# Kernel tuning notes

Measured on AMD Instinct MI355X. Metric: run time of the kernel, lower is better.

## Reference

```python
import jax, jax.numpy as jnp
import numpy as np

B, N, F_IN = 16, 2048, 6
NUM_CLASSES = 16


def _laplacian(x):
    # x: [B,N,F]; Gaussian adjacency from pairwise sq distances, then sym-normalized Laplacian
    sq = jnp.sum(x * x, axis=-1, keepdims=True)            # [B,N,1]
    d2 = sq - 2.0 * jnp.einsum('bnf,bmf->bnm', x, x) + jnp.swapaxes(sq, 1, 2)
    adj = jnp.exp(-d2)                                      # [B,N,N]
    dinv = 1.0 / jnp.sqrt(jnp.sum(adj, axis=-1))            # [B,N]
    return jnp.eye(N, dtype=x.dtype) - adj * dinv[:, :, None] * dinv[:, None, :]


def _cheb(x, L, W, b):
    # Chebyshev conv: W [K,Fin,Fout], recursion x_k = 2 L x_{k-1} - x_{k-2}
    K = W.shape[0]
    x0 = x
    out = jnp.einsum('bnf,fg->bng', x0, W[0])
    if K > 1:
        x1 = jnp.einsum('bnm,bmf->bnf', L, x0)
        out = out + jnp.einsum('bnf,fg->bng', x1, W[1])
        for k in range(2, K):
            x2 = 2.0 * jnp.einsum('bnm,bmf->bnf', L, x1) - x0
            out = out + jnp.einsum('bnf,fg->bng', x2, W[k])
            x0, x1 = x1, x2
    return out + b


def setup_inputs() -> dict:
    key = jax.random.key(0)
    ks = jax.random.split(key, 16)

    def w(k, shape, fan_in):
        return jax.random.normal(k, shape, dtype=jnp.float32) * (1.0 / np.sqrt(fan_in))

    inp = {
        'x': jax.random.normal(ks[0], (B, N, F_IN), dtype=jnp.float32),
        'cat': jax.random.randint(ks[1], (B, 1), 0, NUM_CLASSES),
        'W1': w(ks[2], (6, 22, 128), 22), 'b1': jnp.zeros((128,), jnp.float32),
        'W2': w(ks[3], (5, 128, 512), 128), 'b2': jnp.zeros((512,), jnp.float32),
        'W3': w(ks[4], (3, 512, 1024), 512), 'b3': jnp.zeros((1024,), jnp.float32),
        'fc1_w': w(ks[5], (1024, 512), 1024), 'fc1_b': jnp.zeros((512,), jnp.float32),
        'fc2_w': w(ks[6], (1024, 128), 1024), 'fc2_b': jnp.zeros((128,), jnp.float32),
        'fc3_w': w(ks[7], (128, 50), 128), 'fc3_b': jnp.zeros((50,), jnp.float32),
        'br0': jnp.zeros((1, 1, 128), jnp.float32),
        'br1': jnp.zeros((1, 1, 512), jnp.float32),
        'br2': jnp.zeros((1, 1, 1024), jnp.float32),
        'br3': jnp.zeros((1, 1, 512), jnp.float32),
        'br4': jnp.zeros((1, 1, 128), jnp.float32),
        'br5': jnp.zeros((1, 1, 50), jnp.float32),
    }
    return inp


def reference(x, cat, W1, b1, W2, b2, W3, b3, fc1_w, fc1_b, fc2_w, fc2_b,
              fc3_w, fc3_b, br0, br1, br2, br3, br4, br5):
    L = _laplacian(x)                                        # computed under no_grad in torch
    oh = jax.nn.one_hot(cat[:, 0], NUM_CLASSES, dtype=x.dtype)   # [B,16]
    cat_tiled = jnp.broadcast_to(oh[:, None, :], (x.shape[0], N, NUM_CLASSES))
    h = jnp.concatenate([x, cat_tiled], axis=2)              # [B,N,22]

    h = jax.nn.relu(_cheb(h, L, W1, b1) + br0)               # [B,N,128]
    h = jax.nn.relu(_cheb(h, L, W2, b2) + br1)               # [B,N,512]
    x1 = h
    h = jax.nn.relu(_cheb(h, L, W3, b3) + br2)               # [B,N,1024]

    h = jax.nn.relu(h @ fc1_w + fc1_b + br3)                 # [B,N,512]
    h = jnp.concatenate([h, x1], axis=2)                     # [B,N,1024]
    h = jax.nn.relu(h @ fc2_w + fc2_b + br4)                 # [B,N,128]
    h = jax.nn.relu(h @ fc3_w + fc3_b + br5)                 # [B,N,50]
    return h
```

## Files before the change

kernel.cpp:

```cpp
#include <hip/hip_runtime.h>

#define BB 16
#define NN 2048
#define FIN 6
#define MTOT (BB*NN)

typedef unsigned short u16;
typedef __attribute__((ext_vector_type(8))) short  short8;
typedef __attribute__((ext_vector_type(4))) float  f32x4;

__device__ inline float ldf(const u16* p) {
  unsigned u = ((unsigned)*p) << 16; float f; __builtin_memcpy(&f, &u, 4); return f;
}
__device__ inline u16 tobf(float v) {
  unsigned u; __builtin_memcpy(&u, &v, 4);
  u = (u + 0x7FFFu + ((u >> 16) & 1u)) >> 16;
  return (u16)u;
}
__device__ inline void stf(u16* p, float v) { *p = tobf(v); }

__device__ __forceinline__ void gload16(const u16* g, u16* l) {
  __builtin_amdgcn_global_load_lds(
      (const __attribute__((address_space(1))) void*)g,
      (__attribute__((address_space(3))) void*)l, 16, 0, 0);
}

__global__ __launch_bounds__(256) void k_dpart(const float* __restrict__ x,
                                               float* __restrict__ dsum) {
  __shared__ float xs[512][FIN];
  __shared__ float sqs[512];
  const int b = blockIdx.y;
  const int j0 = blockIdx.z * 512;
  const float* xb = x + (size_t)b * NN * FIN;
  for (int l = threadIdx.x; l < 512 * FIN; l += 256) ((float*)xs)[l] = xb[(size_t)j0 * FIN + l];
  __syncthreads();
  for (int j = threadIdx.x; j < 512; j += 256) {
    float s = 0.f;
#pragma unroll
    for (int f = 0; f < FIN; ++f) { float v = xs[j][f]; s = fmaf(v, v, s); }
    sqs[j] = s;
  }
  __syncthreads();
  const int i = blockIdx.x * 256 + threadIdx.x;
  float xi[FIN];
#pragma unroll
  for (int f = 0; f < FIN; ++f) xi[f] = xb[(size_t)i * FIN + f];
  float sqi = 0.f;
#pragma unroll
  for (int f = 0; f < FIN; ++f) sqi = fmaf(xi[f], xi[f], sqi);
  float a0 = 0.f, a1 = 0.f, a2 = 0.f, a3 = 0.f;
  for (int j = 0; j < 512; j += 4) {
#pragma unroll
    for (int u = 0; u < 4; ++u) {
      const int jj = j + u;
      float dot = 0.f;
#pragma unroll
      for (int f = 0; f < FIN; ++f) dot = fmaf(xs[jj][f], xi[f], dot);
      const float e = __expf(2.f * dot - sqi - sqs[jj]);
      if (u == 0) a0 += e; else if (u == 1) a1 += e; else if (u == 2) a2 += e; else a3 += e;
    }
  }
  atomicAdd(&dsum[b * NN + i], (a0 + a1) + (a2 + a3));
}

__global__ void k_rsq(float* __restrict__ d) {
  const int i = blockIdx.x * 256 + threadIdx.x;
  d[i] = 1.0f / sqrtf(d[i]);
}

__global__ __launch_bounds__(256) void k_lap(const float* __restrict__ x,
                                             const float* __restrict__ dinv,
                                             u16* __restrict__ Lm) {
  const int b = blockIdx.z;
  const int i0 = blockIdx.y * 32;
  const int j0 = blockIdx.x * 256;
  __shared__ float xi[32][FIN];
  __shared__ float di[32];
  const int t = threadIdx.x;
  const float* xb = x + (size_t)b * NN * FIN;
  if (t < 32 * FIN) ((float*)xi)[t] = xb[i0 * FIN + t];
  if (t >= 224) di[t - 224] = dinv[b * NN + i0 + (t - 224)];
  const int j = j0 + t;
  float xj[FIN];
#pragma unroll
  for (int f = 0; f < FIN; ++f) xj[f] = xb[j * FIN + f];
  float sqj = 0.f;
#pragma unroll
  for (int f = 0; f < FIN; ++f) sqj = fmaf(xj[f], xj[f], sqj);
  const float dj = dinv[b * NN + j];
  __syncthreads();
  u16* Lb = Lm + (size_t)b * NN * NN;
#pragma unroll 4
  for (int ii = 0; ii < 32; ++ii) {
    float sqi = 0.f, dot = 0.f;
#pragma unroll
    for (int f = 0; f < FIN; ++f) {
      const float v = xi[ii][f];
      sqi = fmaf(v, v, sqi);
      dot = fmaf(v, xj[f], dot);
    }
    float val = -__expf(2.f * dot - sqi - sqj) * di[ii] * dj;
    if (i0 + ii == j) val += 1.f;
    stf(&Lb[(size_t)(i0 + ii) * NN + j], val);
  }
}

__global__ void k_h0T(const float* __restrict__ x, const int* __restrict__ cat,
                      u16* __restrict__ T1T) {
  const int c = blockIdx.y;
  const int m = blockIdx.x * 256 + threadIdx.x;
  float v;
  if (c < 6) v = x[(size_t)m * 6 + c];
  else v = (cat[m >> 11] == (c - 6)) ? 1.f : 0.f;
  stf(&T1T[(size_t)c * MTOT + m], v);
}

__global__ void k_wt(const float* __restrict__ in, u16* __restrict__ out,
                     int R, int C, int ldo) {
  const int r = blockIdx.x * 256 + threadIdx.x;
  const int c = blockIdx.y;
  if (r < R) stf(&out[(size_t)c * ldo + r], in[(size_t)r * C + c]);
}

__global__ __launch_bounds__(256) void k_actT(const u16* __restrict__ in,
                                              u16* __restrict__ out, int F, int ldo) {
  __shared__ u16 t[64][70];
  const int m0 = blockIdx.x * 64;
  const int f0 = blockIdx.y * 64;
  const int tid = threadIdx.x;
#pragma unroll
  for (int v = 0; v < 4; ++v) {
    const int flat = v * 256 + tid;
    const int fr = flat >> 4;
    const int mq = (flat & 15) * 4;
    ushort4 val = {0, 0, 0, 0};
    if (f0 + fr < F) val = *(const ushort4*)&in[(size_t)(f0 + fr) * MTOT + m0 + mq];
    t[fr][mq + 0] = val.x; t[fr][mq + 1] = val.y;
    t[fr][mq + 2] = val.z; t[fr][mq + 3] = val.w;
  }
  __syncthreads();
#pragma unroll
  for (int v = 0; v < 4; ++v) {
    const int flat = v * 256 + tid;
    const int mr = flat >> 4;
    const int fq = (flat & 15) * 4;
    if (f0 + fq >= F) continue;
    u16* dst = &out[(size_t)(m0 + mr) * ldo + f0 + fq];
    if (f0 + fq + 3 < F) {
      ushort4 o;
      o.x = t[fq + 0][mr]; o.y = t[fq + 1][mr];
      o.z = t[fq + 2][mr]; o.w = t[fq + 3][mr];
      *(ushort4*)dst = o;
    } else {
#pragma unroll
      for (int e = 0; e < 4; ++e)
        if (f0 + fq + e < F) dst[e] = t[fq + e][mr];
    }
  }
}

template <int BM, int BN, int EPI, bool TWOQ, typename OT>
__global__ __launch_bounds__(256) void k_mmL(
    const u16* __restrict__ P, long ldp, int rowsP, long strideP,
    const u16* __restrict__ Q0, long ldq0,
    const u16* __restrict__ Q1, long ldq1, int ksplitT,
    int rowsQ, long strideQ, int K,
    OT* __restrict__ Out, long ldo, long strideO,
    const u16* __restrict__ Prev, float alpha, float beta,
    const float* __restrict__ bias, const float* __restrict__ br, int biasOnI) {
  const int b = blockIdx.z;
  const int i0 = blockIdx.y * BM;
  const int j0 = blockIdx.x * BN;
  const u16* Pb = P + (size_t)b * strideP;
  const u16* Qb0 = Q0 + (size_t)b * strideQ;
  OT* Ob = Out + (size_t)b * strideO;
  const u16* Vb = Prev ? Prev + (size_t)b * strideO : nullptr;

  __shared__ __align__(16) u16 Ps[2][BM * 64];
  __shared__ __align__(16) u16 Qs[2][BN * 64];
  const int tid = threadIdx.x;
  const int lane = tid & 63;
  const int w = tid >> 6;
  const int wr = w >> 1, wc = w & 1;
  constexpr int FI = BM / 32;
  constexpr int FJ = BN / 32;
  constexpr int VP = BM / 32;
  constexpr int VQ = BN / 32;
  const int rl = lane >> 3;
  const int kb = (((lane & 7) ^ rl) << 3);

  const u16* prow[VP];
  bool pok[VP];
#pragma unroll
  for (int v = 0; v < VP; ++v) {
    const int c = w + v * 4;
    const int gr = i0 + c * 8 + rl;
    pok[v] = gr < rowsP;
    prow[v] = Pb + (size_t)gr * ldp + kb;
  }
  const u16* qrow[VQ];
  const u16* qrow1[TWOQ ? VQ : 1];
  bool qok[VQ];
#pragma unroll
  for (int v = 0; v < VQ; ++v) {
    const int c = w + v * 4;
    const int gr = j0 + c * 8 + rl;
    qok[v] = gr < rowsQ;
    qrow[v] = Qb0 + (size_t)gr * ldq0 + kb;
    if (TWOQ) qrow1[v] = Q1 + (size_t)b * strideQ + (size_t)gr * ldq1 + kb;
  }

  f32x4 acc[FI][FJ];
#pragma unroll
  for (int i = 0; i < FI; ++i)
#pragma unroll
    for (int j = 0; j < FJ; ++j) acc[i][j] = (f32x4){0.f, 0.f, 0.f, 0.f};

  auto stage = [&](int t, int buf) {
#pragma unroll
    for (int v = 0; v < VP; ++v)
      if (pok[v]) gload16(prow[v] + t * 64, &Ps[buf][(w + v * 4) * 512]);
    if (TWOQ) {
      const bool r1 = (t >= ksplitT);
      const int tq = r1 ? (t - ksplitT) : t;
#pragma unroll
      for (int v = 0; v < VQ; ++v)
        if (qok[v]) gload16((r1 ? qrow1[v] : qrow[v]) + tq * 64, &Qs[buf][(w + v * 4) * 512]);
    } else {
#pragma unroll
      for (int v = 0; v < VQ; ++v)
        if (qok[v]) gload16(qrow[v] + t * 64, &Qs[buf][(w + v * 4) * 512]);
    }
  };

  auto compute = [&](int buf) {
#pragma unroll
    for (int h = 0; h < 2; ++h) {
      short8 pf[FI], qf[FJ];
#pragma unroll
      for (int i = 0; i < FI; ++i) {
        const int r = wr * (BM / 2) + i * 16 + (lane & 15);
        const int c = (h * 32 + ((lane >> 4) * 8)) ^ ((r & 7) << 3);
        pf[i] = *(const short8*)&Ps[buf][r * 64 + c];
      }
#pragma unroll
      for (int j = 0; j < FJ; ++j) {
        const int r = wc * (BN / 2) + j * 16 + (lane & 15);
        const int c = (h * 32 + ((lane >> 4) * 8)) ^ ((r & 7) << 3);
        qf[j] = *(const short8*)&Qs[buf][r * 64 + c];
      }
#pragma unroll
      for (int i = 0; i < FI; ++i)
#pragma unroll
        for (int j = 0; j < FJ; ++j)
          acc[i][j] = __builtin_amdgcn_mfma_f32_16x16x32_bf16(pf[i], qf[j], acc[i][j], 0, 0, 0);
    }
  };

  const int nt = K >> 6;
  stage(0, 0);
  asm volatile("s_waitcnt vmcnt(0)" ::: "memory");
  __builtin_amdgcn_s_barrier();
  __builtin_amdgcn_sched_barrier(0);
  for (int t = 0; t < nt; ++t) {
    const int cur = t & 1;
    if (t + 1 < nt) stage(t + 1, cur ^ 1);
    compute(cur);
    asm volatile("s_waitcnt vmcnt(0)" ::: "memory");
    __builtin_amdgcn_s_barrier();
    __builtin_amdgcn_sched_barrier(0);
  }

  const int ibase = i0 + wr * (BM / 2);
  const int jbase = j0 + wc * (BN / 2);
#pragma unroll
  for (int j = 0; j < FJ; ++j) {
    const int jj = jbase + j * 16 + (lane & 15);
    if (jj >= rowsQ) continue;
    float bj = 0.f;
    if (EPI == 1 && !biasOnI) bj = bias[jj] + br[jj];
#pragma unroll
    for (int i = 0; i < FI; ++i) {
      const int ii = ibase + i * 16 + ((lane >> 4) << 2);
      f32x4 a = acc[i][j];
      float v[4];
#pragma unroll
      for (int e = 0; e < 4; ++e) {
        float xv = a[e];
        if (EPI == 0) {
          xv *= alpha;
          if (beta != 0.f) xv = fmaf(beta, ldf(&Vb[(size_t)jj * ldo + ii + e]), xv);
        } else {
          float bb = bj;
          if (biasOnI) bb = (ii + e < rowsP) ? (bias[ii + e] + br[ii + e]) : 0.f;
          xv = fmaxf(xv + bb, 0.f);
        }
        v[e] = xv;
      }
      if constexpr (sizeof(OT) == 2) {
        u16* dst = (u16*)&Ob[(size_t)jj * ldo + ii];
        if (ii + 3 < rowsP) {
          ushort4 o; o.x = tobf(v[0]); o.y = tobf(v[1]); o.z = tobf(v[2]); o.w = tobf(v[3]);
          *(ushort4*)dst = o;
        } else {
#pragma unroll
          for (int e = 0; e < 4; ++e) if (ii + e < rowsP) dst[e] = tobf(v[e]);
        }
      } else {
        float* dst = (float*)&Ob[(size_t)jj * ldo + ii];
#pragma unroll
        for (int e = 0; e < 4; ++e) if (ii + e < rowsP) dst[e] = v[e];
      }
    }
  }
}

extern "C" void kernel_launch(void* const* d_in, const int* in_sizes, int n_in,
                              void* d_out, int out_size, void* d_ws, size_t ws_size,
                              hipStream_t stream) {
  const float* x    = (const float*)d_in[0];
  const int*   cat  = (const int*)  d_in[1];
  const float* W1   = (const float*)d_in[2];
  const float* b1   = (const float*)d_in[3];
  const float* W2   = (const float*)d_in[4];
  const float* b2   = (const float*)d_in[5];
  const float* W3   = (const float*)d_in[6];
  const float* b3   = (const float*)d_in[7];
  const float* fc1w = (const float*)d_in[8];
  const float* fc1b = (const float*)d_in[9];
  const float* fc2w = (const float*)d_in[10];
  const float* fc2b = (const float*)d_in[11];
  const float* fc3w = (const float*)d_in[12];
  const float* fc3b = (const float*)d_in[13];
  const float* br0  = (const float*)d_in[14];
  const float* br1  = (const float*)d_in[15];
  const float* br2  = (const float*)d_in[16];
  const float* br3  = (const float*)d_in[17];
  const float* br4  = (const float*)d_in[18];
  const float* br5  = (const float*)d_in[19];

  if (ws_size < 240054784ull) return;

  u16* ws = (u16*)d_ws;
  u16* Wt1p = ws;
  u16* Wt2  = Wt1p + 24576;
  u16* Wt3  = Wt2 + 327680;
  u16* Wtf1 = Wt3 + 1572864;
  u16* Wtf2 = Wtf1 + 524288;
  u16* Wtf3 = Wtf2 + 131072;
  u16* Lbuf = ws + 2586880;
  u16* ACT  = Lbuf + 67108864;

  float* dinv = (float*)ACT;
  u16* T1T   = ACT;
  u16* L1rm  = ACT + 4325376;
  u16* T2T   = ACT;
  u16* L2rm  = ACT + 20971520;
  u16* T3T   = ACT;
  u16* L3rm  = Lbuf;
  u16* h3rm  = ACT;
  u16* fc1o  = ACT + 33554432;
  u16* h5    = ACT;

  const long MT = MTOT;
  const int BIG = 1 << 28;

  hipMemsetAsync(dinv, 0, (size_t)MTOT * 4, stream);
  hipMemsetAsync(Wt1p, 0, 24576 * 2, stream);
  hipMemsetAsync(L1rm, 0, (size_t)MTOT * 192 * 2, stream);

  k_wt<<<dim3(1, 128), 256, 0, stream>>>(W1, Wt1p, 132, 128, 192);
  k_wt<<<dim3(3, 512), 256, 0, stream>>>(W2, Wt2, 640, 512, 640);
  k_wt<<<dim3(6, 1024), 256, 0, stream>>>(W3, Wt3, 1536, 1024, 1536);
  k_wt<<<dim3(4, 512), 256, 0, stream>>>(fc1w, Wtf1, 1024, 512, 1024);
  k_wt<<<dim3(4, 128), 256, 0, stream>>>(fc2w, Wtf2, 1024, 128, 1024);
  k_wt<<<dim3(1, 50), 256, 0, stream>>>(fc3w, Wtf3, 128, 50, 128);

  k_dpart<<<dim3(8, BB, 4), 256, 0, stream>>>(x, dinv);
  k_rsq<<<dim3(MTOT / 256), 256, 0, stream>>>(dinv);
  k_lap<<<dim3(8, 64, BB), 256, 0, stream>>>(x, dinv, Lbuf);

  k_h0T<<<dim3(128, 22), 256, 0, stream>>>(x, cat, T1T);
  {
    const size_t s = (size_t)22 * MT;
    k_mmL<64, 32, 0, false, u16><<<dim3(1, 32, BB), 256, 0, stream>>>(
        Lbuf, NN, NN, (long)NN * NN, T1T, MT, nullptr, 0, BIG, 22, NN,
        NN, T1T + s, MT, NN, nullptr, 1.f, 0.f, nullptr, nullptr, 0);
    for (int k = 2; k < 6; ++k)
      k_mmL<64, 32, 0, false, u16><<<dim3(1, 32, BB), 256, 0, stream>>>(
          Lbuf, NN, NN, (long)NN * NN, T1T + (k - 1) * s, MT, nullptr, 0, BIG, 22, NN,
          NN, T1T + k * s, MT, NN, T1T + (k - 2) * s, 2.f, -1.f, nullptr, nullptr, 0);
  }
  k_actT<<<dim3(512, 3), 256, 0, stream>>>(T1T, L1rm, 132, 192);
  k_mmL<128, 128, 1, false, u16><<<dim3(1, 256, 1), 256, 0, stream>>>(
      L1rm, 192, MTOT, 0, Wt1p, 192, nullptr, 0, BIG, 128, 0,
      192, T2T, MT, 0, nullptr, 0.f, 0.f, b1, br0, 0);

  {
    const size_t s = (size_t)128 * MT;
    k_mmL<64, 128, 0, false, u16><<<dim3(1, 32, BB), 256, 0, stream>>>(
        Lbuf, NN, NN, (long)NN * NN, T2T, MT, nullptr, 0, BIG, 128, NN,
        NN, T2T + s, MT, NN, nullptr, 1.f, 0.f, nullptr, nullptr, 0);
    for (int k = 2; k < 5; ++k)
      k_mmL<64, 128, 0, false, u16><<<dim3(1, 32, BB), 256, 0, stream>>>(
          Lbuf, NN, NN, (long)NN * NN, T2T + (k - 1) * s, MT, nullptr, 0, BIG, 128, NN,
          NN, T2T + k * s, MT, NN, T2T + (k - 2) * s, 2.f, -1.f, nullptr, nullptr, 0);
  }
  k_actT<<<dim3(512, 10), 256, 0, stream>>>(T2T, L2rm, 640, 640);
  k_mmL<128, 128, 1, false, u16><<<dim3(4, 256, 1), 256, 0, stream>>>(
      L2rm, 640, MTOT, 0, Wt2, 640, nullptr, 0, BIG, 512, 0,
      640, T3T, MT, 0, nullptr, 0.f, 0.f, b2, br1, 0);

  {
    const size_t s = (size_t)512 * MT;
    k_mmL<128, 128, 0, false, u16><<<dim3(4, 16, BB), 256, 0, stream>>>(
        Lbuf, NN, NN, (long)NN * NN, T3T, MT, nullptr, 0, BIG, 512, NN,
        NN, T3T + s, MT, NN, nullptr, 1.f, 0.f, nullptr, nullptr, 0);
    k_mmL<128, 128, 0, false, u16><<<dim3(4, 16, BB), 256, 0, stream>>>(
        Lbuf, NN, NN, (long)NN * NN, T3T + s, MT, nullptr, 0, BIG, 512, NN,
        NN, T3T + 2 * s, MT, NN, T3T, 2.f, -1.f, nullptr, nullptr, 0);
  }
  k_actT<<<dim3(512, 24), 256, 0, stream>>>(T3T, L3rm, 1536, 1536);
  k_mmL<128, 128, 1, false, u16><<<dim3(256, 8, 1), 256, 0, stream>>>(
      Wt3, 1536, 1024, 0, L3rm, 1536, nullptr, 0, BIG, MTOT, 0,
      1536, h3rm, 1024, 0, nullptr, 0.f, 0.f, b3, br2, 1);

  k_mmL<128, 128, 1, false, u16><<<dim3(256, 4, 1), 256, 0, stream>>>(
      Wtf1, 1024, 512, 0, h3rm, 1024, nullptr, 0, BIG, MTOT, 0,
      1024, fc1o, 512, 0, nullptr, 0.f, 0.f, fc1b, br3, 1);
  k_mmL<64, 128, 1, true, u16><<<dim3(256, 2, 1), 256, 0, stream>>>(
      Wtf2, 1024, 128, 0, fc1o, 512, L3rm, 1536, 8, MTOT, 0,
      1024, h5, 128, 0, nullptr, 0.f, 0.f, fc2b, br4, 1);
  k_mmL<64, 128, 1, false, float><<<dim3(256, 1, 1), 256, 0, stream>>>(
      Wtf3, 128, 50, 0, h5, 128, nullptr, 0, BIG, MTOT, 0,
      128, (float*)d_out, 50, 0, nullptr, 0.f, 0.f, fc3b, br5, 1);
}
```

Baseline: 1.141 ms.

## Prefetch two K-tiles ahead with partial vmcnt waits in GEMM loop

Restructures the double-buffered GEMM main loop so two tiles are in flight. After computing a buffer, the kernel barriers, issues the load for tile t+2 into that buffer, and waits only until the older tile's loads retire (vmcnt(LP)) rather than draining all loads. Out-of-range row guards are replaced by clamping row pointers, which removes branches around the async loads so the per-thread load count stays fixed for the vmcnt accounting. This adds a second barrier per iteration, and the clamped rows load duplicate data that must be ignored in the epilogue.

```diff
diff --git a/kernel.cpp b/kernel.cpp
--- a/kernel.cpp
+++ b/kernel.cpp
@@ -23,6 +23,12 @@
   __builtin_amdgcn_global_load_lds(
       (const __attribute__((address_space(1))) void*)g,
       (__attribute__((address_space(3))) void*)l, 16, 0, 0);
+}
+
+template <int N>
+__device__ __forceinline__ void wait_vmcnt() {
+  __builtin_amdgcn_s_waitcnt(0xF70 | N);
+  __builtin_amdgcn_sched_barrier(0);
 }
 
 __global__ __launch_bounds__(256) void k_dpart(const float* __restrict__ x,
@@ -186,26 +192,25 @@
   constexpr int FJ = BN / 32;
   constexpr int VP = BM / 32;
   constexpr int VQ = BN / 32;
+  constexpr int LP = VP + VQ;
   const int rl = lane >> 3;
   const int kb = (((lane & 7) ^ rl) << 3);
 
   const u16* prow[VP];
-  bool pok[VP];
 #pragma unroll
   for (int v = 0; v < VP; ++v) {
     const int c = w + v * 4;
-    const int gr = i0 + c * 8 + rl;
-    pok[v] = gr < rowsP;
+    int gr = i0 + c * 8 + rl;
+    if (gr >= rowsP) gr = rowsP - 1;
     prow[v] = Pb + (size_t)gr * ldp + kb;
   }
   const u16* qrow[VQ];
   const u16* qrow1[TWOQ ? VQ : 1];
-  bool qok[VQ];
 #pragma unroll
   for (int v = 0; v < VQ; ++v) {
     const int c = w + v * 4;
-    const int gr = j0 + c * 8 + rl;
-    qok[v] = gr < rowsQ;
+    int gr = j0 + c * 8 + rl;
+    if (gr >= rowsQ) gr = rowsQ - 1;
     qrow[v] = Qb0 + (size_t)gr * ldq0 + kb;
     if (TWOQ) qrow1[v] = Q1 + (size_t)b * strideQ + (size_t)gr * ldq1 + kb;
   }
@@ -219,17 +224,17 @@
   auto stage = [&](int t, int buf) {
 #pragma unroll
     for (int v = 0; v < VP; ++v)
-      if (pok[v]) gload16(prow[v] + t * 64, &Ps[buf][(w + v * 4) * 512]);
+      gload16(prow[v] + t * 64, &Ps[buf][(w + v * 4) * 512]);
     if (TWOQ) {
       const bool r1 = (t >= ksplitT);
       const int tq = r1 ? (t - ksplitT) : t;
 #pragma unroll
       for (int v = 0; v < VQ; ++v)
-        if (qok[v]) gload16((r1 ? qrow1[v] : qrow[v]) + tq * 64, &Qs[buf][(w + v * 4) * 512]);
+        gload16((r1 ? qrow1[v] : qrow[v]) + tq * 64, &Qs[buf][(w + v * 4) * 512]);
     } else {
 #pragma unroll
       for (int v = 0; v < VQ; ++v)
-        if (qok[v]) gload16(qrow[v] + t * 64, &Qs[buf][(w + v * 4) * 512]);
+        gload16(qrow[v] + t * 64, &Qs[buf][(w + v * 4) * 512]);
     }
   };
 
@@ -259,14 +264,21 @@
 
   const int nt = K >> 6;
   stage(0, 0);
-  asm volatile("s_waitcnt vmcnt(0)" ::: "memory");
+  stage(1, 1);
+  wait_vmcnt<LP>();
   __builtin_amdgcn_s_barrier();
   __builtin_amdgcn_sched_barrier(0);
   for (int t = 0; t < nt; ++t) {
     const int cur = t & 1;
-    if (t + 1 < nt) stage(t + 1, cur ^ 1);
     compute(cur);
-    asm volatile("s_waitcnt vmcnt(0)" ::: "memory");
+    __builtin_amdgcn_s_barrier();
+    __builtin_amdgcn_sched_barrier(0);
+    if (t + 2 < nt) {
+      stage(t + 2, cur);
+      wait_vmcnt<LP>();
+    } else {
+      wait_vmcnt<0>();
+    }
     __builtin_amdgcn_s_barrier();
     __builtin_amdgcn_sched_barrier(0);
   }
```

Result: no change. 1.155 ms (+1.2%).
